# Kernel tuning notes

Hardware: AMD Instinct MI355X
Metric: run time of the kernel (lower is better)

## Reference

```python
import jax, jax.numpy as jnp
import numpy as np

HIDDEN = 1024
HEADS = 16
MEM = 2
D_H = HIDDEN // HEADS
NEG = -1.0e9


def setup_inputs() -> dict:
    key = jax.random.key(0)
    ks = jax.random.split(key, 8)
    B, M, N = 16, 512, 512
    s = 1.0 / np.sqrt(HIDDEN)
    return {
        "x": jax.random.normal(ks[0], (B, M, HIDDEN), dtype=jnp.float32),
        "y": jax.random.normal(ks[1], (B, N, HIDDEN), dtype=jnp.float32),
        "mask_x": jax.random.randint(ks[2], (B, M), 0, 2, dtype=jnp.int64),
        "mask_y": jax.random.randint(ks[3], (B, N), 0, 2, dtype=jnp.int64),
        "Wx": jax.random.normal(ks[4], (HIDDEN, HIDDEN), dtype=jnp.float32) * s,
        "Wy": jax.random.normal(ks[5], (HIDDEN, HIDDEN), dtype=jnp.float32) * s,
        "x_memory": jax.random.normal(ks[6], (MEM, HIDDEN), dtype=jnp.float32),
        "y_memory": jax.random.normal(ks[7], (MEM, HIDDEN), dtype=jnp.float32),
    }


def _project(t, mem, W):
    # prepend memory tokens, then linear (torch Linear: t @ W^T), split heads
    B = t.shape[0]
    t_mem = jnp.concatenate([jnp.broadcast_to(mem[None], (B, MEM, HIDDEN)), t], axis=1)
    proj = t_mem @ W.T
    proj = proj.reshape(B, t_mem.shape[1], HEADS, D_H)
    return t_mem, proj


def reference(x, y, mask_x, mask_y, Wx, Wy, x_memory, y_memory):
    B = x.shape[0]
    mem_mask = jnp.ones((B, MEM), dtype=mask_x.dtype)
    mx = jnp.concatenate([mem_mask, mask_x], axis=1)  # [B, M+MEM]
    my = jnp.concatenate([mem_mask, mask_y], axis=1)  # [B, N+MEM]

    X_mem, X_proj = _project(x, x_memory, Wx)  # [B,Mm,H], [B,Mm,heads,d_h]
    Y_mem, Y_proj = _project(y, y_memory, Wy)

    # affinity: [B, heads, Mm, Nm]
    aff = jnp.einsum("bmhd,bnhd->bhmn", X_proj, Y_proj)
    aff = jnp.where(mx[:, None, :, None] == 0, NEG, aff)
    aff = jnp.where(my[:, None, None, :] == 0, NEG, aff)

    attn_X = jnp.mean(jax.nn.softmax(aff, axis=2), axis=1)  # [B, Mm, Nm]
    attn_Y = jnp.mean(jax.nn.softmax(aff, axis=3), axis=1)  # [B, Mm, Nm]

    X_in_Y = jnp.einsum("bmn,bmh->bnh", attn_X, X_mem)[:, MEM:, :]  # [B, N, H]
    Y_in_X = jnp.einsum("bmn,bnh->bmh", attn_Y, Y_mem)[:, MEM:, :]  # [B, M, H]
    return X_in_Y, Y_in_X
```

## Files before the change

kernel.cpp:

```cpp
#include <hip/hip_runtime.h>

#define B_   16
#define SEQ  512
#define MM   514
#define HID  1024
#define NH   16
#define DH   64
#define KP   544
#define MTOT (B_ * MM)
#define UNI  (1.0f/514.0f)

typedef unsigned short us;
typedef __attribute__((ext_vector_type(4))) float f32x4;
typedef __attribute__((ext_vector_type(8))) short short8;
typedef __attribute__((ext_vector_type(8))) _Float16 half8;

__device__ __forceinline__ us f2bf(float f) {
  unsigned int u = __float_as_uint(f);
  u = (u + 0x7FFFu + ((u >> 16) & 1u)) >> 16;
  return (us)u;
}
__device__ __forceinline__ float bf2f(us h) {
  return __uint_as_float(((unsigned int)h) << 16);
}
__device__ __forceinline__ us f2h(float f) {
  _Float16 h = (_Float16)f;
  return *(us*)&h;
}
__device__ __forceinline__ unsigned cvt_pk_bf16(float lo, float hi) {
  unsigned d;
  asm("v_cvt_pk_bf16_f32 %0, %1, %2" : "=v"(d) : "v"(lo), "v"(hi));
  return d;
}

__global__ __launch_bounds__(256) void prepack(
    const float* __restrict__ x, const float* __restrict__ y,
    const float* __restrict__ xm, const float* __restrict__ ym,
    const float* __restrict__ Wx, const float* __restrict__ Wy,
    us* __restrict__ Abf, us* __restrict__ Wbf) {
  const int tid = threadIdx.x;
  const int row = blockIdx.x * 4 + (tid >> 6);
  const int path = blockIdx.y;
  const int lane = tid & 63;
  const float* src;
  us* dst;
  if (row < MTOT) {
    const int gb = row / MM, gt = row - gb * MM;
    const float* tin = path ? y : x;
    const float* mv  = path ? ym : xm;
    src = (gt < 2) ? (mv + (size_t)gt * HID)
                   : (tin + ((size_t)(gb * SEQ + gt - 2)) * HID);
    dst = Abf + ((size_t)(path * MTOT + row)) * HID;
  } else {
    const int o = row - MTOT;
    src = (path ? Wy : Wx) + (size_t)o * HID;
    dst = Wbf + ((size_t)(path * HID + o)) * HID;
  }
  const float* s = src + lane * 16;
  f32x4 v0 = *(const f32x4*)(s);
  f32x4 v1 = *(const f32x4*)(s + 4);
  f32x4 v2 = *(const f32x4*)(s + 8);
  f32x4 v3 = *(const f32x4*)(s + 12);
  uint4 w0, w1;
  w0.x = cvt_pk_bf16(v0[0], v0[1]);  w0.y = cvt_pk_bf16(v0[2], v0[3]);
  w0.z = cvt_pk_bf16(v1[0], v1[1]);  w0.w = cvt_pk_bf16(v1[2], v1[3]);
  w1.x = cvt_pk_bf16(v2[0], v2[1]);  w1.y = cvt_pk_bf16(v2[2], v2[3]);
  w1.z = cvt_pk_bf16(v3[0], v3[1]);  w1.w = cvt_pk_bf16(v3[2], v3[3]);
  *(uint4*)(dst + lane * 16)     = w0;
  *(uint4*)(dst + lane * 16 + 8) = w1;
}

__global__ __launch_bounds__(256) void proj_fused2(
    const us* __restrict__ Abf, const us* __restrict__ Wbf,
    us* __restrict__ Px, us* __restrict__ Py) {
  const int lin = blockIdx.x + 8 * (blockIdx.y + 65 * blockIdx.z);
  const int work = (lin & 7) * 130 + (lin >> 3);
  const int path = (work >= 520) ? 1 : 0;
  const int wrem = work - path * 520;
  const int mt = wrem >> 3, nt = wrem & 7;
  us* P = path ? Py : Px;
  const us* Ab = Abf + (size_t)path * MTOT * HID;
  const us* Wb = Wbf + (size_t)path * HID * HID;

  __shared__ __align__(16) us As[128 * 40];
  __shared__ __align__(16) us Bs[128 * 40];
  const int tid = threadIdx.x;
  const int lane = tid & 63, wave = tid >> 6;
  const int c = lane & 15, q = lane >> 4;
  const int wr = wave >> 1, wc = wave & 1;

  const int srow = tid >> 1, sch = (tid & 1) * 16;
  const int grow = mt * 128 + srow;
  const us* asrc = (grow < MTOT) ? (Ab + (size_t)grow * HID + sch) : nullptr;
  const us* bsrc = Wb + (size_t)(nt * 128 + srow) * HID + sch;
  us* wAp = &As[srow * 40 + sch];
  us* wBp = &Bs[srow * 40 + sch];
  const us* rA = &As[(wr * 64 + c) * 40 + q * 8];
  const us* rB = &Bs[(wc * 64 + c) * 40 + q * 8];

  f32x4 acc[4][4];
#pragma unroll
  for (int i = 0; i < 4; i++)
#pragma unroll
    for (int j = 0; j < 4; j++) acc[i][j] = (f32x4){0.f, 0.f, 0.f, 0.f};

  uint4 z4 = {0u, 0u, 0u, 0u};
  uint4 pa0 = z4, pa1 = z4, pb0, pb1;
  if (asrc) { pa0 = *(const uint4*)asrc; pa1 = *(const uint4*)(asrc + 8); }
  pb0 = *(const uint4*)bsrc; pb1 = *(const uint4*)(bsrc + 8);

  for (int kk = 0; kk < HID; kk += 32) {
    __syncthreads();
    *(uint4*)wAp       = pa0;
    *(uint4*)(wAp + 8) = pa1;
    *(uint4*)wBp       = pb0;
    *(uint4*)(wBp + 8) = pb1;
    __syncthreads();
    if (kk + 32 < HID) {
      if (asrc) {
        pa0 = *(const uint4*)(asrc + kk + 32);
        pa1 = *(const uint4*)(asrc + kk + 32 + 8);
      }
      pb0 = *(const uint4*)(bsrc + kk + 32);
      pb1 = *(const uint4*)(bsrc + kk + 32 + 8);
    }
    short8 a[4], bb[4];
#pragma unroll
    for (int i = 0; i < 4; i++) a[i] = *(const short8*)(rA + i * 16 * 40);
#pragma unroll
    for (int j = 0; j < 4; j++) bb[j] = *(const short8*)(rB + j * 16 * 40);
#pragma unroll
    for (int i = 0; i < 4; i++)
#pragma unroll
      for (int j = 0; j < 4; j++)
        acc[i][j] = __builtin_amdgcn_mfma_f32_16x16x32_bf16(a[i], bb[j], acc[i][j], 0, 0, 0);
  }
#pragma unroll
  for (int i = 0; i < 4; i++) {
#pragma unroll
    for (int r = 0; r < 4; r++) {
      int gr = mt * 128 + wr * 64 + i * 16 + q * 4 + r;
      if (gr < MTOT) {
        size_t rb = (size_t)gr * HID;
#pragma unroll
        for (int j = 0; j < 4; j++)
          P[rb + nt * 128 + wc * 64 + j * 16 + c] = f2bf(acc[i][j][r]);
      }
    }
  }
}

__device__ __forceinline__ void stage_bf(
    us* Xs, const us* P, int b, int r0, int h, int tid) {
#pragma unroll
  for (int i = 0; i < 2; i++) {
    int idx = tid + i * 256;
    int row = idx >> 3, qq = idx & 7;
    *(uint4*)&Xs[row * 72 + qq * 8] =
        *(const uint4*)(P + ((size_t)(b * MM + min(r0 + row, MM - 1))) * HID + h * DH + qq * 8);
  }
}

__global__ __launch_bounds__(512) void sums_v3(
    const us* __restrict__ Px, const us* __restrict__ Py,
    const int* __restrict__ mx, const int* __restrict__ my,
    float* __restrict__ Sums) {
  const int lin = blockIdx.x;
  const int work = (lin & 7) * 160 + (lin >> 3);
  const int b = work / 80;
  const int rem = work - b * 80;
  const int h = rem / 5;
  const int nc = rem - h * 5;
  const int n0 = nc * 128;
  __shared__ __align__(16) us Ys[128 * 72];
  __shared__ __align__(16) us Xs[64 * 72];
  __shared__ float cS[128];
  __shared__ int myS[128];
  __shared__ int mxS[576];
  const int tid = threadIdx.x;
  const int lane = tid & 63, wave = tid >> 6;
  const int c = lane & 15, q = lane >> 4;
  const int strip = wave & 3, cgrp = wave >> 2;

  for (int i = tid; i < 128; i += 512) {
    cS[i] = 0.f;
    int n = n0 + i;
    myS[i] = (n >= MM) ? 0 : ((n < 2) ? 1 : my[b * SEQ + n - 2]);
  }
  for (int i = tid; i < 576; i += 512)
    mxS[i] = (i >= MM) ? 0 : ((i < 2) ? 1 : mx[b * SEQ + i - 2]);
  {
#pragma unroll
    for (int it = 0; it < 2; it++) {
      int idx = tid + it * 512;
      int row = idx >> 3, qq = idx & 7;
      int grow = min(n0 + row, MM - 1);
      *(uint4*)&Ys[row * 72 + qq * 8] =
          *(const uint4*)(Py + ((size_t)(b * MM + grow)) * HID + h * DH + qq * 8);
    }
  }
  __syncthreads();

  const size_t base = ((size_t)(b * NH + h)) * MM;
  const size_t COLOFF = (size_t)B_ * NH * MM;

  for (int mt = 0; mt < 9; mt++) {
    {
      const int row8 = tid >> 3, qq = tid & 7;
      int grow = min(mt * 64 + row8, MM - 1);
      *(uint4*)&Xs[row8 * 72 + qq * 8] =
          *(const uint4*)(Px + ((size_t)(b * MM + grow)) * HID + h * DH + qq * 8);
    }
    __syncthreads();
    short8 a0 = *(const short8*)&Xs[(strip * 16 + c) * 72 + q * 8];
    short8 a1 = *(const short8*)&Xs[(strip * 16 + c) * 72 + q * 8 + 32];
    int rm[4];
#pragma unroll
    for (int r = 0; r < 4; r++) rm[r] = mxS[mt * 64 + strip * 16 + q * 4 + r];
    float rowp[4] = {0.f, 0.f, 0.f, 0.f};
#pragma unroll
    for (int ss = 0; ss < 4; ss++) {
      int nloc = cgrp * 64 + ss * 16 + c;
      short8 b0 = *(const short8*)&Ys[nloc * 72 + q * 8];
      short8 b1 = *(const short8*)&Ys[nloc * 72 + q * 8 + 32];
      f32x4 av = (f32x4){0.f, 0.f, 0.f, 0.f};
      av = __builtin_amdgcn_mfma_f32_16x16x32_bf16(a0, b0, av, 0, 0, 0);
      av = __builtin_amdgcn_mfma_f32_16x16x32_bf16(a1, b1, av, 0, 0, 0);
      int cmv = myS[nloc];
      float colp = 0.f;
#pragma unroll
      for (int r = 0; r < 4; r++) {
        float e = (rm[r] && cmv) ? __expf(av[r]) : 0.f;
        rowp[r] += e;
        colp += e;
      }
      colp += __shfl_xor(colp, 16);
      colp += __shfl_xor(colp, 32);
      if (q == 0) atomicAdd(&cS[nloc], colp);
    }
#pragma unroll
    for (int d = 1; d < 16; d <<= 1)
#pragma unroll
      for (int r = 0; r < 4; r++) rowp[r] += __shfl_xor(rowp[r], d, 16);
    if (c == 0) {
#pragma unroll
      for (int r = 0; r < 4; r++) {
        int m = mt * 64 + strip * 16 + q * 4 + r;
        if (m < MM) atomicAdd(&Sums[base + m], rowp[r]);
      }
    }
    __syncthreads();
  }
  for (int i = tid; i < 128; i += 512) {
    int n = n0 + i;
    if (n < MM) atomicAdd(&Sums[COLOFF + base + n], cS[i]);
  }
}

__global__ __launch_bounds__(256) void inv_kernel(float* __restrict__ Sums) {
  int i = blockIdx.x * 256 + threadIdx.x;
  if (i < 2 * B_ * NH * MM) {
    float s = Sums[i];
    Sums[i] = (s > 0.f) ? (1.f / s) : -1.f;
  }
}

__global__ __launch_bounds__(256) void attn_swz(
    const us* __restrict__ Px, const us* __restrict__ Py,
    const int* __restrict__ mx, const int* __restrict__ my,
    const float* __restrict__ Inv,
    us* __restrict__ attnXT, us* __restrict__ attnY) {
  const int lin = blockIdx.x;
  const int work = (lin & 7) * 162 + (lin >> 3);
  const int b = work / 81;
  const int rem = work - b * 81;
  const int mt = rem / 9;
  const int nt = rem - mt * 9;
  __shared__ __align__(16) us Xs[64 * 72];
  __shared__ __align__(16) us Ys[64 * 72];
  const int tid = threadIdx.x;
  const int lane = tid & 63, wave = tid >> 6;
  const int c = lane & 15, q = lane >> 4;
  const size_t COLOFF = (size_t)B_ * NH * MM;

  int mreg[4], rm[4], ncol[4], cm[4];
#pragma unroll
  for (int r = 0; r < 4; r++) {
    mreg[r] = mt * 64 + wave * 16 + q * 4 + r;
    rm[r] = (mreg[r] >= MM) ? 0 : ((mreg[r] < 2) ? 1 : mx[b * SEQ + mreg[r] - 2]);
  }
#pragma unroll
  for (int s = 0; s < 4; s++) {
    ncol[s] = nt * 64 + s * 16 + c;
    cm[s] = (ncol[s] >= MM) ? 0 : ((ncol[s] < 2) ? 1 : my[b * SEQ + ncol[s] - 2]);
  }

  float aX[4][4], aY[4][4];
#pragma unroll
  for (int s = 0; s < 4; s++)
#pragma unroll
    for (int r = 0; r < 4; r++) { aX[s][r] = 0.f; aY[s][r] = 0.f; }

  for (int h = 0; h < NH; h++) {
    __syncthreads();
    stage_bf(Xs, Px, b, mt * 64, h, tid);
    stage_bf(Ys, Py, b, nt * 64, h, tid);
    __syncthreads();
    short8 a0 = *(const short8*)&Xs[(wave * 16 + c) * 72 + q * 8];
    short8 a1 = *(const short8*)&Xs[(wave * 16 + c) * 72 + q * 8 + 32];
    const size_t base = ((size_t)(b * NH + h)) * MM;
    float invR[4];
#pragma unroll
    for (int r = 0; r < 4; r++) invR[r] = Inv[base + min(mreg[r], MM - 1)];
#pragma unroll
    for (int s = 0; s < 4; s++) {
      float invC = Inv[COLOFF + base + min(ncol[s], MM - 1)];
      short8 b0 = *(const short8*)&Ys[(s * 16 + c) * 72 + q * 8];
      short8 b1 = *(const short8*)&Ys[(s * 16 + c) * 72 + q * 8 + 32];
      f32x4 av = (f32x4){0.f, 0.f, 0.f, 0.f};
      av = __builtin_amdgcn_mfma_f32_16x16x32_bf16(a0, b0, av, 0, 0, 0);
      av = __builtin_amdgcn_mfma_f32_16x16x32_bf16(a1, b1, av, 0, 0, 0);
#pragma unroll
      for (int r = 0; r < 4; r++) {
        float e = (rm[r] && cm[s]) ? __expf(av[r]) : 0.f;
        aY[s][r] += (invR[r] < 0.f) ? UNI : e * invR[r];
        aX[s][r] += (invC < 0.f) ? UNI : e * invC;
      }
    }
  }
#pragma unroll
  for (int s = 0; s < 4; s++) {
    if (ncol[s] < MM) {
      us* xrow = attnXT + ((size_t)(b * MM + ncol[s])) * KP;
      if (mreg[3] < MM) {
        uint2 w;
        w.x = (unsigned)f2h(aX[s][0] * 0.0625f) | ((unsigned)f2h(aX[s][1] * 0.0625f) << 16);
        w.y = (unsigned)f2h(aX[s][2] * 0.0625f) | ((unsigned)f2h(aX[s][3] * 0.0625f) << 16);
        *(uint2*)&xrow[mreg[0]] = w;
      } else {
#pragma unroll
        for (int r = 0; r < 4; r++)
          if (mreg[r] < MM) xrow[mreg[r]] = f2h(aX[s][r] * 0.0625f);
      }
#pragma unroll
      for (int r = 0; r < 4; r++)
        if (mreg[r] < MM)
          attnY[((size_t)(b * MM + mreg[r])) * KP + ncol[s]] = f2h(aY[s][r] * 0.0625f);
    }
  }
}

__global__ __launch_bounds__(256) void transpose_fused(
    const float* __restrict__ x, const float* __restrict__ y,
    const float* __restrict__ xm, const float* __restrict__ ym,
    us* __restrict__ XTx, us* __restrict__ XTy) {
  const int kt = blockIdx.x, ot = blockIdx.y;
  const int b = blockIdx.z & 15, path = blockIdx.z >> 4;
  const float* tin  = path ? y  : x;
  const float* mvec = path ? ym : xm;
  us* XT            = path ? XTy : XTx;
  __shared__ __align__(16) us T[64 * 40];
  const int tid = threadIdx.x;
  {
    const int row = tid >> 3;
    const int col8 = (tid & 7) * 8;
    const int kg = kt * 32 + row;
    const float* src = (kg < 2) ? (mvec + (size_t)kg * HID + ot * 64 + col8)
                     : (kg < MM) ? (tin + ((size_t)(b * SEQ + kg - 2)) * HID + ot * 64 + col8)
                                 : nullptr;
    f32x4 v0 = (f32x4){0.f, 0.f, 0.f, 0.f};
    f32x4 v1 = (f32x4){0.f, 0.f, 0.f, 0.f};
    if (src) { v0 = *(const f32x4*)src; v1 = *(const f32x4*)(src + 4); }
#pragma unroll
    for (int j = 0; j < 4; j++) T[(col8 + j) * 40 + row] = f2h(v0[j]);
#pragma unroll
    for (int j = 0; j < 4; j++) T[(col8 + 4 + j) * 40 + row] = f2h(v1[j]);
  }
  __syncthreads();
  const int orow = tid >> 2, kc = (tid & 3) * 8;
  uint4 w = *(const uint4*)&T[orow * 40 + kc];
  *(uint4*)&XT[((size_t)(b * HID + ot * 64 + orow)) * KP + kt * 32 + kc] = w;
}

__global__ __launch_bounds__(256) void outg_fused(
    const us* __restrict__ A0, const us* __restrict__ A1,
    const us* __restrict__ XTx, const us* __restrict__ XTy,
    float* __restrict__ outp) {
  const int ot = blockIdx.x, rt = blockIdx.y;
  const int b = blockIdx.z & 15, path = blockIdx.z >> 4;
  const us* A  = path ? A1 : A0;
  const us* XT = path ? XTy : XTx;
  float* op = outp + (path ? (size_t)B_ * SEQ * HID : 0);
  const int r0 = rt * 128, o0 = ot * 128;
  __shared__ __align__(16) us As[128 * 40];
  __shared__ __align__(16) us Bs[128 * 40];
  const int tid = threadIdx.x;
  const int lane = tid & 63, wave = tid >> 6;
  const int c = lane & 15, q = lane >> 4;
  const int wr = wave >> 1, wc = wave & 1;

  const int srow = tid >> 2, sch = (tid & 3) * 8;
  const us* gA0 = A + ((size_t)(b * MM + 2 + r0 + srow)) * KP + sch;
  const us* gA1 = gA0 + (size_t)64 * KP;
  const us* gB0 = XT + ((size_t)(b * HID + o0 + srow)) * KP + sch;
  const us* gB1 = gB0 + (size_t)64 * KP;
  us* wA0 = &As[srow * 40 + sch];
  us* wA1 = wA0 + 64 * 40;
  us* wB0 = &Bs[srow * 40 + sch];
  us* wB1 = wB0 + 64 * 40;

  f32x4 acc[4][4];
#pragma unroll
  for (int i = 0; i < 4; i++)
#pragma unroll
    for (int j = 0; j < 4; j++) acc[i][j] = (f32x4){0.f, 0.f, 0.f, 0.f};

  const us* rA = &As[(wr * 64 + c) * 40 + q * 8];
  const us* rB = &Bs[(wc * 64 + c) * 40 + q * 8];

  uint4 pA0 = *(const uint4*)gA0;
  uint4 pA1 = *(const uint4*)gA1;
  uint4 pB0 = *(const uint4*)gB0;
  uint4 pB1 = *(const uint4*)gB1;

  for (int kk = 0; kk < KP; kk += 32) {
    __syncthreads();
    *(uint4*)wA0 = pA0;
    *(uint4*)wA1 = pA1;
    *(uint4*)wB0 = pB0;
    *(uint4*)wB1 = pB1;
    __syncthreads();
    if (kk + 32 < KP) {
      pA0 = *(const uint4*)(gA0 + kk + 32);
      pA1 = *(const uint4*)(gA1 + kk + 32);
      pB0 = *(const uint4*)(gB0 + kk + 32);
      pB1 = *(const uint4*)(gB1 + kk + 32);
    }
    half8 a[4], bb[4];
#pragma unroll
    for (int i = 0; i < 4; i++) a[i] = *(const half8*)(rA + i * 16 * 40);
#pragma unroll
    for (int j = 0; j < 4; j++) bb[j] = *(const half8*)(rB + j * 16 * 40);
#pragma unroll
    for (int i = 0; i < 4; i++)
#pragma unroll
      for (int j = 0; j < 4; j++)
        acc[i][j] = __builtin_amdgcn_mfma_f32_16x16x32_f16(a[i], bb[j], acc[i][j], 0, 0, 0);
  }
#pragma unroll
  for (int i = 0; i < 4; i++) {
#pragma unroll
    for (int rr = 0; rr < 4; rr++) {
      int r = r0 + wr * 64 + i * 16 + q * 4 + rr;
      size_t rowbase = ((size_t)(b * SEQ + r)) * HID;
#pragma unroll
      for (int j = 0; j < 4; j++)
        op[rowbase + o0 + wc * 64 + j * 16 + c] = acc[i][j][rr];
    }
  }
}

__global__ __launch_bounds__(256) void attn_mfma_old(
    const us* __restrict__ Px, const us* __restrict__ Py,
    const int* __restrict__ mx, const int* __restrict__ my,
    const float* __restrict__ Inv,
    us* __restrict__ attnX, us* __restrict__ attnY,
    const int doX, const int doY) {
  const int nt = blockIdx.x, mt = blockIdx.y, b = blockIdx.z;
  __shared__ __align__(16) us Xs[64 * 72];
  __shared__ __align__(16) us Ys[64 * 72];
  const int tid = threadIdx.x;
  const int lane = tid & 63, wave = tid >> 6;
  const int c = lane & 15, q = lane >> 4;
  const size_t COLOFF = (size_t)B_ * NH * MM;

  int mreg[4], rm[4], ncol[4], cm[4];
#pragma unroll
  for (int r = 0; r < 4; r++) {
    mreg[r] = mt * 64 + wave * 16 + q * 4 + r;
    rm[r] = (mreg[r] >= MM) ? 0 : ((mreg[r] < 2) ? 1 : mx[b * SEQ + mreg[r] - 2]);
  }
#pragma unroll
  for (int s = 0; s < 4; s++) {
    ncol[s] = nt * 64 + s * 16 + c;
    cm[s] = (ncol[s] >= MM) ? 0 : ((ncol[s] < 2) ? 1 : my[b * SEQ + ncol[s] - 2]);
  }

  float aX[4][4], aY[4][4];
#pragma unroll
  for (int s = 0; s < 4; s++)
#pragma unroll
    for (int r = 0; r < 4; r++) { aX[s][r] = 0.f; aY[s][r] = 0.f; }

  for (int h = 0; h < NH; h++) {
    __syncthreads();
    stage_bf(Xs, Px, b, mt * 64, h, tid);
    stage_bf(Ys, Py, b, nt * 64, h, tid);
    __syncthreads();
    short8 a0 = *(const short8*)&Xs[(wave * 16 + c) * 72 + q * 8];
    short8 a1 = *(const short8*)&Xs[(wave * 16 + c) * 72 + q * 8 + 32];
    const size_t base = ((size_t)(b * NH + h)) * MM;
    float invR[4];
#pragma unroll
    for (int r = 0; r < 4; r++) invR[r] = Inv[base + min(mreg[r], MM - 1)];
#pragma unroll
    for (int s = 0; s < 4; s++) {
      float invC = Inv[COLOFF + base + min(ncol[s], MM - 1)];
      short8 b0 = *(const short8*)&Ys[(s * 16 + c) * 72 + q * 8];
      short8 b1 = *(const short8*)&Ys[(s * 16 + c) * 72 + q * 8 + 32];
      f32x4 av = (f32x4){0.f, 0.f, 0.f, 0.f};
      av = __builtin_amdgcn_mfma_f32_16x16x32_bf16(a0, b0, av, 0, 0, 0);
      av = __builtin_amdgcn_mfma_f32_16x16x32_bf16(a1, b1, av, 0, 0, 0);
#pragma unroll
      for (int r = 0; r < 4; r++) {
        float e = (rm[r] && cm[s]) ? __expf(av[r]) : 0.f;
        aY[s][r] += (invR[r] < 0.f) ? UNI : e * invR[r];
        aX[s][r] += (invC < 0.f) ? UNI : e * invC;
      }
    }
  }
#pragma unroll
  for (int s = 0; s < 4; s++) {
#pragma unroll
    for (int r = 0; r < 4; r++) {
      if (mreg[r] < MM && ncol[s] < MM) {
        size_t idx = ((size_t)(b * MM + mreg[r])) * MM + ncol[s];
        if (doX) attnX[idx] = f2bf(aX[s][r] * 0.0625f);
        if (doY) attnY[idx] = f2bf(aY[s][r] * 0.0625f);
      }
    }
  }
}

__global__ __launch_bounds__(256) void outg_kernel(
    const us* __restrict__ attn, const float* __restrict__ tin,
    const float* __restrict__ mvec, float* __restrict__ outp, const int trans) {
  const int otile = blockIdx.x, rtile = blockIdx.y, b = blockIdx.z;
  __shared__ __align__(16) float Ss[32 * 132];
  __shared__ __align__(16) float Ms[32 * 132];
  const int tid = threadIdx.x;
  const int r0 = rtile * 128, o0 = otile * 128;

  float acc[8][8];
#pragma unroll
  for (int i = 0; i < 8; i++)
#pragma unroll
    for (int j = 0; j < 8; j++) acc[i][j] = 0.f;

  for (int kk = 0; kk < 544; kk += 32) {
    __syncthreads();
    if (trans) {
      int rq = (tid & 31) * 4;
      int kr = tid >> 5;
#pragma unroll
      for (int kb = 0; kb < 32; kb += 8) {
        int k = kr + kb;
        int kg = kk + k;
        if (kg < MM) {
          const us* src = attn + ((size_t)(b * MM + kg)) * MM + 2 + r0 + rq;
          Ss[k * 132 + rq + 0] = bf2f(src[0]);
          Ss[k * 132 + rq + 1] = bf2f(src[1]);
          Ss[k * 132 + rq + 2] = bf2f(src[2]);
          Ss[k * 132 + rq + 3] = bf2f(src[3]);
        } else {
          Ss[k * 132 + rq + 0] = 0.f;
          Ss[k * 132 + rq + 1] = 0.f;
          Ss[k * 132 + rq + 2] = 0.f;
          Ss[k * 132 + rq + 3] = 0.f;
        }
      }
    } else {
      int r = tid >> 1;
      int kh = (tid & 1) * 16;
      const us* src = attn + ((size_t)(b * MM + 2 + r0 + r)) * MM;
#pragma unroll
      for (int j = 0; j < 16; j++) {
        int k = kh + j;
        int kg = kk + k;
        Ss[k * 132 + r] = (kg < MM) ? bf2f(src[kg]) : 0.f;
      }
    }
    {
      int k = tid >> 3;
      int oq = (tid & 7) * 16;
      int kg = kk + k;
      const float* mr = (kg < 2) ? (mvec + (size_t)kg * HID)
                      : (kg < MM) ? (tin + ((size_t)(b * SEQ + kg - 2)) * HID)
                                  : nullptr;
#pragma unroll
      for (int qq = 0; qq < 4; qq++) {
        f32x4 v = (f32x4){0.f, 0.f, 0.f, 0.f};
        if (mr) v = *(const f32x4*)(mr + o0 + oq + qq * 4);
        *(f32x4*)&Ms[k * 132 + oq + qq * 4] = v;
      }
    }
    __syncthreads();
    const int ty = tid >> 4, tx = tid & 15;
    for (int k = 0; k < 32; k++) {
      f32x4 s0 = *(const f32x4*)&Ss[k * 132 + ty * 4];
      f32x4 s1 = *(const f32x4*)&Ss[k * 132 + 64 + ty * 4];
      f32x4 m0 = *(const f32x4*)&Ms[k * 132 + tx * 4];
      f32x4 m1 = *(const f32x4*)&Ms[k * 132 + 64 + tx * 4];
#pragma unroll
      for (int i = 0; i < 4; i++) {
#pragma unroll
        for (int j = 0; j < 4; j++) {
          acc[i][j]         += s0[i] * m0[j];
          acc[i][j + 4]     += s0[i] * m1[j];
          acc[i + 4][j]     += s1[i] * m0[j];
          acc[i + 4][j + 4] += s1[i] * m1[j];
        }
      }
    }
  }
  const int ty = tid >> 4, tx = tid & 15;
#pragma unroll
  for (int ri = 0; ri < 2; ri++) {
#pragma unroll
    for (int i = 0; i < 4; i++) {
      int r = r0 + ri * 64 + ty * 4 + i;
      size_t rowbase = ((size_t)(b * SEQ + r)) * HID;
#pragma unroll
      for (int oi = 0; oi < 2; oi++) {
        int o = o0 + oi * 64 + tx * 4;
        f32x4 v;
#pragma unroll
        for (int j = 0; j < 4; j++) v[j] = acc[ri * 4 + i][oi * 4 + j];
        *(f32x4*)&outp[rowbase + o] = v;
      }
    }
  }
}

extern "C" void kernel_launch(void* const* d_in, const int* in_sizes, int n_in,
                              void* d_out, int out_size, void* d_ws, size_t ws_size,
                              hipStream_t stream) {
  const float* x  = (const float*)d_in[0];
  const float* y  = (const float*)d_in[1];
  const int* mask_x = (const int*)d_in[2];
  const int* mask_y = (const int*)d_in[3];
  const float* Wx = (const float*)d_in[4];
  const float* Wy = (const float*)d_in[5];
  const float* xm = (const float*)d_in[6];
  const float* ym = (const float*)d_in[7];
  float* out = (float*)d_out;

  const size_t szSums = (size_t)2 * B_ * NH * MM * 4;
  const size_t szP    = (size_t)B_ * MM * HID * 2;
  const size_t szAtt  = (size_t)B_ * MM * MM * 2;
  const size_t szAttP = (size_t)B_ * MM * KP * 2;
  const size_t szXT   = (size_t)B_ * HID * KP * 2;
  const size_t R_off  = szSums + 2 * szAttP;
  const size_t needNew = R_off + 2 * szXT;

  char* ws = (char*)d_ws;

  us* Abf = (us*)d_out;
  us* Wbf = (us*)d_out + (size_t)2 * MTOT * HID;

  if (ws_size >= needNew) {
    float* Sums = (float*)ws;
    us* A0  = (us*)(ws + szSums);
    us* A1  = (us*)(ws + szSums + szAttP);
    us* Px  = (us*)(ws + R_off);
    us* Py  = (us*)(ws + R_off + szP);
    us* XTx = (us*)(ws + R_off);
    us* XTy = (us*)(ws + R_off + szXT);

    prepack<<<dim3((MTOT + HID) / 4, 2), 256, 0, stream>>>(x, y, xm, ym, Wx, Wy, Abf, Wbf);
    proj_fused2<<<dim3(8, 65, 2), 256, 0, stream>>>(Abf, Wbf, Px, Py);
    hipMemsetAsync(Sums, 0, szSums, stream);
    hipMemsetAsync(A0, 0, 2 * szAttP, stream);
    sums_v3<<<dim3(1280), 512, 0, stream>>>(Px, Py, mask_x, mask_y, Sums);
    inv_kernel<<<dim3((2 * B_ * NH * MM + 255) / 256), 256, 0, stream>>>(Sums);
    attn_swz<<<dim3(1296), 256, 0, stream>>>(Px, Py, mask_x, mask_y, Sums, A0, A1);
    transpose_fused<<<dim3(17, 16, 32), 256, 0, stream>>>(x, y, xm, ym, XTx, XTy);
    outg_fused<<<dim3(8, 4, 32), 256, 0, stream>>>(A0, A1, XTx, XTy, out);
    return;
  }

  const int dual = (ws_size >= szSums + 2 * szP + 2 * szAtt) ? 1 : 0;
  float* Sums = (float*)(ws);
  us* Px = (us*)(ws + szSums);
  us* Py = (us*)(ws + szSums + szP);
  us* A0 = (us*)(ws + szSums + 2 * szP);
  us* A1 = dual ? (us*)(ws + szSums + 2 * szP + szAtt) : A0;

  prepack<<<dim3((MTOT + HID) / 4, 2), 256, 0, stream>>>(x, y, xm, ym, Wx, Wy, Abf, Wbf);
  proj_fused2<<<dim3(8, 65, 2), 256, 0, stream>>>(Abf, Wbf, Px, Py);
  hipMemsetAsync(Sums, 0, szSums, stream);
  sums_v3<<<dim3(1280), 512, 0, stream>>>(Px, Py, mask_x, mask_y, Sums);
  inv_kernel<<<dim3((2 * B_ * NH * MM + 255) / 256), 256, 0, stream>>>(Sums);

  if (dual) {
    attn_mfma_old<<<dim3(9, 9, 16), 256, 0, stream>>>(Px, Py, mask_x, mask_y, Sums, A0, A1, 1, 1);
    outg_kernel<<<dim3(8, 4, 16), 256, 0, stream>>>(A0, x, xm, out, 1);
    outg_kernel<<<dim3(8, 4, 16), 256, 0, stream>>>(A1, y, ym, out + (size_t)B_ * SEQ * HID, 0);
  } else {
    attn_mfma_old<<<dim3(9, 9, 16), 256, 0, stream>>>(Px, Py, mask_x, mask_y, Sums, A0, A0, 1, 0);
    outg_kernel<<<dim3(8, 4, 16), 256, 0, stream>>>(A0, x, xm, out, 1);
    attn_mfma_old<<<dim3(9, 9, 16), 256, 0, stream>>>(Px, Py, mask_x, mask_y, Sums, A0, A0, 0, 1);
    outg_kernel<<<dim3(8, 4, 16), 256, 0, stream>>>(A0, y, ym, out + (size_t)B_ * SEQ * HID, 0);
  }
}
```

Before: 372.1 us.

## Double-buffer X tiles and replace atomics with register/shared partial sums in sums kernel

The sums kernel now double-buffers the X tile in shared memory and prefetches the next tile into registers while the current one is computed, which removes one barrier per iteration. Column sums stay in registers across all M tiles and are reduced once at the end through shared memory. Per-row partials are stored to shared memory and flushed with one global atomic per row per block, replacing the per-tile shared and global atomics. Shared memory use goes up, which may lower occupancy, and the column sums are now written directly since each block owns its column chunk.

```diff
diff --git a/kernel.cpp b/kernel.cpp
--- a/kernel.cpp
+++ b/kernel.cpp
@@ -161,7 +161,7 @@
   }
 }
 
-__global__ __launch_bounds__(512) void sums_v3(
+__global__ __launch_bounds__(512) void sums_v4(
     const us* __restrict__ Px, const us* __restrict__ Py,
     const int* __restrict__ mx, const int* __restrict__ my,
     float* __restrict__ Sums) {
@@ -173,17 +173,18 @@
   const int nc = rem - h * 5;
   const int n0 = nc * 128;
   __shared__ __align__(16) us Ys[128 * 72];
-  __shared__ __align__(16) us Xs[64 * 72];
-  __shared__ float cS[128];
+  __shared__ __align__(16) us Xs[2][64 * 72];
+  __shared__ float cS2[4][128];
+  __shared__ float rS2[2][576];
   __shared__ int myS[128];
   __shared__ int mxS[576];
   const int tid = threadIdx.x;
   const int lane = tid & 63, wave = tid >> 6;
   const int c = lane & 15, q = lane >> 4;
   const int strip = wave & 3, cgrp = wave >> 2;
+  const int row8 = tid >> 3, qq = tid & 7;
 
   for (int i = tid; i < 128; i += 512) {
-    cS[i] = 0.f;
     int n = n0 + i;
     myS[i] = (n >= MM) ? 0 : ((n < 2) ? 1 : my[b * SEQ + n - 2]);
   }
@@ -193,27 +194,37 @@
 #pragma unroll
     for (int it = 0; it < 2; it++) {
       int idx = tid + it * 512;
-      int row = idx >> 3, qq = idx & 7;
+      int row = idx >> 3, q8 = idx & 7;
       int grow = min(n0 + row, MM - 1);
-      *(uint4*)&Ys[row * 72 + qq * 8] =
-          *(const uint4*)(Py + ((size_t)(b * MM + grow)) * HID + h * DH + qq * 8);
-    }
+      *(uint4*)&Ys[row * 72 + q8 * 8] =
+          *(const uint4*)(Py + ((size_t)(b * MM + grow)) * HID + h * DH + q8 * 8);
+    }
+  }
+  {
+    int grow = min(row8, MM - 1);
+    *(uint4*)&Xs[0][row8 * 72 + qq * 8] =
+        *(const uint4*)(Px + ((size_t)(b * MM + grow)) * HID + h * DH + qq * 8);
   }
   __syncthreads();
 
   const size_t base = ((size_t)(b * NH + h)) * MM;
   const size_t COLOFF = (size_t)B_ * NH * MM;
 
+  int myReg[4];
+#pragma unroll
+  for (int ss = 0; ss < 4; ss++) myReg[ss] = myS[cgrp * 64 + ss * 16 + c];
+
+  float colAcc[4] = {0.f, 0.f, 0.f, 0.f};
+
   for (int mt = 0; mt < 9; mt++) {
-    {
-      const int row8 = tid >> 3, qq = tid & 7;
-      int grow = min(mt * 64 + row8, MM - 1);
-      *(uint4*)&Xs[row8 * 72 + qq * 8] =
-          *(const uint4*)(Px + ((size_t)(b * MM + grow)) * HID + h * DH + qq * 8);
-    }
-    __syncthreads();
-    short8 a0 = *(const short8*)&Xs[(strip * 16 + c) * 72 + q * 8];
-    short8 a1 = *(const short8*)&Xs[(strip * 16 + c) * 72 + q * 8 + 32];
+    const us* xb = &Xs[mt & 1][0];
+    uint4 nx = {0u, 0u, 0u, 0u};
+    if (mt + 1 < 9) {
+      int grow = min((mt + 1) * 64 + row8, MM - 1);
+      nx = *(const uint4*)(Px + ((size_t)(b * MM + grow)) * HID + h * DH + qq * 8);
+    }
+    short8 a0 = *(const short8*)&xb[(strip * 16 + c) * 72 + q * 8];
+    short8 a1 = *(const short8*)&xb[(strip * 16 + c) * 72 + q * 8 + 32];
     int rm[4];
 #pragma unroll
     for (int r = 0; r < 4; r++) rm[r] = mxS[mt * 64 + strip * 16 + q * 4 + r];
@@ -226,17 +237,12 @@
       f32x4 av = (f32x4){0.f, 0.f, 0.f, 0.f};
       av = __builtin_amdgcn_mfma_f32_16x16x32_bf16(a0, b0, av, 0, 0, 0);
       av = __builtin_amdgcn_mfma_f32_16x16x32_bf16(a1, b1, av, 0, 0, 0);
-      int cmv = myS[nloc];
-      float colp = 0.f;
 #pragma unroll
       for (int r = 0; r < 4; r++) {
-        float e = (rm[r] && cmv) ? __expf(av[r]) : 0.f;
+        float e = (rm[r] && myReg[ss]) ? __expf(av[r]) : 0.f;
         rowp[r] += e;
-        colp += e;
-      }
-      colp += __shfl_xor(colp, 16);
-      colp += __shfl_xor(colp, 32);
-      if (q == 0) atomicAdd(&cS[nloc], colp);
+        colAcc[ss] += e;
+      }
     }
 #pragma unroll
     for (int d = 1; d < 16; d <<= 1)
@@ -244,16 +250,32 @@
       for (int r = 0; r < 4; r++) rowp[r] += __shfl_xor(rowp[r], d, 16);
     if (c == 0) {
 #pragma unroll
-      for (int r = 0; r < 4; r++) {
-        int m = mt * 64 + strip * 16 + q * 4 + r;
-        if (m < MM) atomicAdd(&Sums[base + m], rowp[r]);
-      }
-    }
-    __syncthreads();
-  }
+      for (int r = 0; r < 4; r++)
+        rS2[cgrp][mt * 64 + strip * 16 + q * 4 + r] = rowp[r];
+    }
+    if (mt + 1 < 9)
+      *(uint4*)&Xs[(mt + 1) & 1][row8 * 72 + qq * 8] = nx;
+    __syncthreads();
+  }
+
+#pragma unroll
+  for (int ss = 0; ss < 4; ss++) {
+    colAcc[ss] += __shfl_xor(colAcc[ss], 16);
+    colAcc[ss] += __shfl_xor(colAcc[ss], 32);
+  }
+  if (q == 0) {
+#pragma unroll
+    for (int ss = 0; ss < 4; ss++)
+      cS2[strip][cgrp * 64 + ss * 16 + c] = colAcc[ss];
+  }
+  __syncthreads();
   for (int i = tid; i < 128; i += 512) {
     int n = n0 + i;
-    if (n < MM) atomicAdd(&Sums[COLOFF + base + n], cS[i]);
+    if (n < MM)
+      Sums[COLOFF + base + n] = cS2[0][i] + cS2[1][i] + cS2[2][i] + cS2[3][i];
+  }
+  for (int i = tid; i < 576; i += 512) {
+    if (i < MM) atomicAdd(&Sums[base + i], rS2[0][i] + rS2[1][i]);
   }
 }
 
@@ -671,7 +693,7 @@
     proj_fused2<<<dim3(8, 65, 2), 256, 0, stream>>>(Abf, Wbf, Px, Py);
     hipMemsetAsync(Sums, 0, szSums, stream);
     hipMemsetAsync(A0, 0, 2 * szAttP, stream);
-    sums_v3<<<dim3(1280), 512, 0, stream>>>(Px, Py, mask_x, mask_y, Sums);
+    sums_v4<<<dim3(1280), 512, 0, stream>>>(Px, Py, mask_x, mask_y, Sums);
     inv_kernel<<<dim3((2 * B_ * NH * MM + 255) / 256), 256, 0, stream>>>(Sums);
     attn_swz<<<dim3(1296), 256, 0, stream>>>(Px, Py, mask_x, mask_y, Sums, A0, A1);
     transpose_fused<<<dim3(17, 16, 32), 256, 0, stream>>>(x, y, xm, ym, XTx, XTy);
@@ -689,7 +711,7 @@
   prepack<<<dim3((MTOT + HID) / 4, 2), 256, 0, stream>>>(x, y, xm, ym, Wx, Wy, Abf, Wbf);
   proj_fused2<<<dim3(8, 65, 2), 256, 0, stream>>>(Abf, Wbf, Px, Py);
   hipMemsetAsync(Sums, 0, szSums, stream);
-  sums_v3<<<dim3(1280), 512, 0, stream>>>(Px, Py, mask_x, mask_y, Sums);
+  sums_v4<<<dim3(1280), 512, 0, stream>>>(Px, Py, mask_x, mask_y, Sums);
   inv_kernel<<<dim3((2 * B_ * NH * MM + 255) / 256), 256, 0, stream>>>(Sums);
 
   if (dual) {
```

New measurement: 349.4 us. 6.1% less time.
